# Kernel optimization log

Measured on AMD Instinct MI355X. Metric: run time of the kernel, lower is better.

## Reference

```python
import jax, jax.numpy as jnp
import numpy as np

NB, NG = 100000, 20000   # bus / gen node counts
D, H = 64, 64            # input feat dim, hidden dim
EL, EX = 1000000, 200000 # line edges, gen<->bus edges
OUT = 16


def setup_inputs() -> dict:
    key = jax.random.key(0)
    ks = jax.random.split(key, 28)

    def nrm(k, shp, scale):
        return jax.random.normal(k, shp, jnp.float32) * scale

    w = 0.05  # small weight scale to keep activations tame over stacked layers
    inp = {
        "x_bus": nrm(ks[0], (NB, D), 1.0),
        "x_gen": nrm(ks[1], (NG, D), 1.0),
        "line_src": jax.random.randint(ks[2], (EL,), 0, NB, jnp.int32),
        "line_dst": jax.random.randint(ks[3], (EL,), 0, NB, jnp.int32),
        "g2b_src": jax.random.randint(ks[4], (EX,), 0, NG, jnp.int32),
        "g2b_dst": jax.random.randint(ks[5], (EX,), 0, NB, jnp.int32),
        "b2g_src": jax.random.randint(ks[6], (EX,), 0, NB, jnp.int32),
        "b2g_dst": jax.random.randint(ks[7], (EX,), 0, NG, jnp.int32),
    }
    i = 8
    for l in range(2):
        din = D if l == 0 else H
        for name in ["W_self_bus", "W_self_gen", "W_line", "W_g2b", "W_b2g"]:
            inp[f"{name}_{l}"] = nrm(ks[i], (din, H), w); i += 1
        inp[f"b_self_bus_{l}"] = jnp.zeros((H,), jnp.float32)
        inp[f"b_self_gen_{l}"] = jnp.zeros((H,), jnp.float32)
    inp["W_h"] = nrm(ks[i], (2 * H, H), w); i += 1
    inp["b_h"] = jnp.zeros((H,), jnp.float32)
    inp["W_o"] = nrm(ks[i], (H, OUT), w); i += 1
    inp["b_o"] = jnp.zeros((OUT,), jnp.float32)
    return inp


def _mean_aggr(msg_src, src, dst, n_dst):
    # transform-at-source already applied; gather then mean-scatter to dst nodes
    m = msg_src[src]  # [E, H]
    s = jax.ops.segment_sum(m, dst, num_segments=n_dst)
    c = jax.ops.segment_sum(jnp.ones(dst.shape, m.dtype), dst, num_segments=n_dst)
    return s / jnp.maximum(c, 1.0)[:, None]


def reference(x_bus, x_gen, line_src, line_dst, g2b_src, g2b_dst, b2g_src, b2g_dst,
              W_self_bus_0, W_self_gen_0, W_line_0, W_g2b_0, W_b2g_0,
              b_self_bus_0, b_self_gen_0,
              W_self_bus_1, W_self_gen_1, W_line_1, W_g2b_1, W_b2g_1,
              b_self_bus_1, b_self_gen_1,
              W_h, b_h, W_o, b_o):
    layers = [
        (W_self_bus_0, b_self_bus_0, W_self_gen_0, b_self_gen_0, W_line_0, W_g2b_0, W_b2g_0),
        (W_self_bus_1, b_self_bus_1, W_self_gen_1, b_self_gen_1, W_line_1, W_g2b_1, W_b2g_1),
    ]
    hb, hg = x_bus, x_gen
    nb, ng = hb.shape[0], hg.shape[0]
    for (Wsb, bsb, Wsg, bsg, Wl, Wg2b, Wb2g) in layers:
        m_line = _mean_aggr(hb @ Wl, line_src, line_dst, nb)   # bus -> bus
        m_g2b = _mean_aggr(hg @ Wg2b, g2b_src, g2b_dst, nb)    # gen -> bus
        m_b2g = _mean_aggr(hb @ Wb2g, b2g_src, b2g_dst, ng)    # bus -> gen
        new_hb = jax.nn.relu(hb @ Wsb + bsb + m_line + m_g2b)
        new_hg = jax.nn.relu(hg @ Wsg + bsg + m_b2g)
        hb, hg = new_hb, new_hg
    # sum-pool each node type, concat, 2-layer MLP head
    g = jnp.concatenate([jnp.sum(hb, axis=0), jnp.sum(hg, axis=0)], axis=-1)
    return jax.nn.relu(g @ W_h + b_h) @ W_o + b_o
```

## Files before the change

kernel.cpp:

```cpp
#include <hip/hip_runtime.h>

#define NB 100000
#define NG 20000
#define EL 1000000
#define EX 200000
#define NSEG (2 * NB + NG)
#define NE (EL + 2 * EX)
#define WROW 72
#define WMAT (64 * WROW)
#define AST 200
#define FPB 128
#define PSEG (NSEG / 8)
#define CAPL 40
#define CAPG 16
#define CAPB 40

typedef __attribute__((ext_vector_type(8))) short bf16x8;
typedef __attribute__((ext_vector_type(4))) float f32x4;

static __device__ __forceinline__ int uni(int x) { return __builtin_amdgcn_readfirstlane(x); }

static __device__ __forceinline__ unsigned short f2bf(float x) {
    unsigned u = __float_as_uint(x);
    u += 0x7FFF + ((u >> 16) & 1);
    return (unsigned short)(u >> 16);
}
static __device__ __forceinline__ float bf2f(unsigned short s) {
    return __uint_as_float(((unsigned)s) << 16);
}

__global__ void cvt_kernel(const float* __restrict__ src, unsigned short* __restrict__ dst, int n) {
    int i = (blockIdx.x * blockDim.x + threadIdx.x) * 4;
    if (i < n) {
        float4 f = *(const float4*)(src + i);
        ushort4 u = { f2bf(f.x), f2bf(f.y), f2bf(f.z), f2bf(f.w) };
        *(ushort4*)(dst + i) = u;
    }
}

__global__ __launch_bounds__(256) void fill_bucket_kernel(
    const int* __restrict__ ls, const int* __restrict__ ld,
    const int* __restrict__ gs, const int* __restrict__ gd,
    const int* __restrict__ bs, const int* __restrict__ bd,
    int* __restrict__ cnt, int* __restrict__ bktL,
    int* __restrict__ bktG, int* __restrict__ bktB)
{
    const int p = blockIdx.x & 7;
    const int q = blockIdx.x >> 3;
    const int lo = p * PSEG;
    const int hi = lo + PSEG;
    for (int i = q * 256 + threadIdx.x; i < NE; i += FPB * 256) {
        int src, seg, cap;
        int* dst;
        if (i < EL) {
            src = ls[i]; int d = ld[i];
            seg = d; dst = bktL + (size_t)d * CAPL; cap = CAPL;
        } else if (i < EL + EX) {
            src = gs[i - EL]; int d = gd[i - EL];
            seg = NB + d; dst = bktG + (size_t)d * CAPG; cap = CAPG;
        } else {
            src = bs[i - EL - EX]; int d = bd[i - EL - EX];
            seg = 2 * NB + d; dst = bktB + (size_t)d * CAPB; cap = CAPB;
        }
        if (seg >= lo && seg < hi) {
            int pos = atomicAdd(&cnt[seg], 1);
            if (pos < cap) dst[pos] = src;
        }
    }
}

struct WPrep { const float* src[10]; unsigned short* dst[10]; };
__global__ __launch_bounds__(256) void wprep_kernel(WPrep p) {
    const float* __restrict__ s = p.src[blockIdx.x];
    unsigned short* __restrict__ d = p.dst[blockIdx.x];
    for (int idx = threadIdx.x; idx < 4096; idx += 256) {
        int k = idx >> 6, nn = idx & 63;
        d[nn * WROW + k] = f2bf(s[idx]);
    }
}

static __device__ __forceinline__ float seg_mean_bkt(const unsigned short* __restrict__ h,
                                                     const int* __restrict__ bkt,
                                                     int cnt, int cap, int lane) {
    float s = 0.f;
    const int n = min(cnt, cap);
    int e = 0;
    for (; e + 8 <= n; e += 8) {
        int i0 = bkt[e],     i1 = bkt[e + 1], i2 = bkt[e + 2], i3 = bkt[e + 3];
        int i4 = bkt[e + 4], i5 = bkt[e + 5], i6 = bkt[e + 6], i7 = bkt[e + 7];
        float v0 = bf2f(h[(size_t)i0 * 64 + lane]), v1 = bf2f(h[(size_t)i1 * 64 + lane]);
        float v2 = bf2f(h[(size_t)i2 * 64 + lane]), v3 = bf2f(h[(size_t)i3 * 64 + lane]);
        float v4 = bf2f(h[(size_t)i4 * 64 + lane]), v5 = bf2f(h[(size_t)i5 * 64 + lane]);
        float v6 = bf2f(h[(size_t)i6 * 64 + lane]), v7 = bf2f(h[(size_t)i7 * 64 + lane]);
        s += ((v0 + v1) + (v2 + v3)) + ((v4 + v5) + (v6 + v7));
    }
    for (; e + 2 <= n; e += 2) {
        int i0 = bkt[e], i1 = bkt[e + 1];
        s += bf2f(h[(size_t)i0 * 64 + lane]) + bf2f(h[(size_t)i1 * 64 + lane]);
    }
    if (e < n) s += bf2f(h[(size_t)bkt[e] * 64 + lane]);
    return s / fmaxf((float)cnt, 1.f);
}

__global__ __launch_bounds__(256) void combine_fused_kernel(
    const unsigned short* __restrict__ hb, const unsigned short* __restrict__ hg,
    const int* __restrict__ cnt,
    const int* __restrict__ bktL, const int* __restrict__ bktG, const int* __restrict__ bktB,
    const unsigned short* __restrict__ WtB, const unsigned short* __restrict__ WtG,
    const float* __restrict__ biasB, const float* __restrict__ biasG,
    unsigned short* __restrict__ outB, unsigned short* __restrict__ outG,
    float* __restrict__ pool, int gbBus)
{
    __shared__ __attribute__((aligned(16))) unsigned short Atile[32 * AST];
    __shared__ float pred[64];
    const int t = threadIdx.x;
    const bool isBus = blockIdx.x < gbBus;
    const int bb = isBus ? blockIdx.x : blockIdx.x - gbBus;
    const int base = bb * 32;
    const int n = isBus ? NB : NG;
    const int nmat = isBus ? 3 : 2;
    const unsigned short* __restrict__ h = isBus ? hb : hg;
    const unsigned short* __restrict__ Wt = isBus ? WtB : WtG;
    const float* __restrict__ bias = isBus ? biasB : biasG;

    if (pool != nullptr && t < 64) pred[t] = 0.f;

#pragma unroll
    for (int i = 0; i < 2; ++i) {
        int flat = i * 1024 + t * 4;
        int r = flat >> 6, c = flat & 63;
        bool ok = (base + r) < n;
        ushort4 z = {0, 0, 0, 0};
        size_t g = (size_t)(base + r) * 64 + c;
        *(ushort4*)&Atile[r * AST + c] = ok ? *(const ushort4*)(h + g) : z;
    }

    const int lane = t & 63;
    const int w = t >> 6;
    for (int r8 = 0; r8 < 8; ++r8) {
        const int r = w * 8 + r8;
        const int row = uni(base + r);
        float vA = 0.f, vB = 0.f;
        if (row < n) {
            if (isBus) {
                int cA = uni(cnt[row]);
                vA = seg_mean_bkt(hb, bktL + (size_t)row * CAPL, cA, CAPL, lane);
                int cB = uni(cnt[NB + row]);
                vB = seg_mean_bkt(hg, bktG + (size_t)row * CAPG, cB, CAPG, lane);
            } else {
                int cA = uni(cnt[2 * NB + row]);
                vA = seg_mean_bkt(hb, bktB + (size_t)row * CAPB, cA, CAPB, lane);
            }
        }
        Atile[r * AST + 64 + lane] = f2bf(vA);
        if (isBus) Atile[r * AST + 128 + lane] = f2bf(vB);
    }
    __syncthreads();

    const int rg = w & 1;
    const int cp = w >> 1;
    const int l15 = lane & 15;
    const int q = lane >> 4;
    f32x4 acc[2];
    acc[0] = (f32x4){0.f, 0.f, 0.f, 0.f};
    acc[1] = (f32x4){0.f, 0.f, 0.f, 0.f};

    const int ksteps = nmat * 2;
    for (int ks = 0; ks < ksteps; ++ks) {
        bf16x8 av = *(const bf16x8*)&Atile[(rg * 16 + l15) * AST + ks * 32 + q * 8];
#pragma unroll
        for (int cc = 0; cc < 2; ++cc) {
            int c = cp * 2 + cc;
            bf16x8 bv = *(const bf16x8*)&Wt[(ks >> 1) * WMAT + (c * 16 + l15) * WROW + (ks & 1) * 32 + q * 8];
            acc[cc] = __builtin_amdgcn_mfma_f32_16x16x32_bf16(av, bv, acc[cc], 0, 0, 0);
        }
    }

    if (pool == nullptr) {
        unsigned short* __restrict__ out = isBus ? outB : outG;
#pragma unroll
        for (int cc = 0; cc < 2; ++cc) {
            const int col = (cp * 2 + cc) * 16 + l15;
            const float bv = bias[col];
#pragma unroll
            for (int reg = 0; reg < 4; ++reg) {
                int row = base + rg * 16 + q * 4 + reg;
                if (row < n) out[(size_t)row * 64 + col] = f2bf(fmaxf(acc[cc][reg] + bv, 0.f));
            }
        }
    } else {
        float* __restrict__ pdst = isBus ? pool : pool + 64;
#pragma unroll
        for (int cc = 0; cc < 2; ++cc) {
            const int col = (cp * 2 + cc) * 16 + l15;
            const float bv = bias[col];
            float s = 0.f;
#pragma unroll
            for (int reg = 0; reg < 4; ++reg) {
                int row = base + rg * 16 + q * 4 + reg;
                if (row < n) s += fmaxf(acc[cc][reg] + bv, 0.f);
            }
            atomicAdd(&pred[col], s);
        }
        __syncthreads();
        if (t < 64) atomicAdd(&pdst[t], pred[t]);
    }
}

__global__ void head_kernel(const float* __restrict__ pool,
                            const float* __restrict__ Wh, const float* __restrict__ bh,
                            const float* __restrict__ Wo, const float* __restrict__ bo,
                            float* __restrict__ out)
{
    __shared__ float g[128];
    __shared__ float hid[64];
    int t = threadIdx.x;
    g[t] = pool[t];
    __syncthreads();
    if (t < 64) {
        float a = bh[t];
        for (int i = 0; i < 128; ++i) a += g[i] * Wh[i * 64 + t];
        hid[t] = fmaxf(a, 0.f);
    }
    __syncthreads();
    if (t < 16) {
        float a = bo[t];
        for (int j = 0; j < 64; ++j) a += hid[j] * Wo[j * 16 + t];
        out[t] = a;
    }
}

extern "C" void kernel_launch(void* const* d_in, const int* in_sizes, int n_in,
                              void* d_out, int out_size, void* d_ws, size_t ws_size,
                              hipStream_t stream)
{
    const float* x_bus   = (const float*)d_in[0];
    const float* x_gen   = (const float*)d_in[1];
    const int* line_src  = (const int*)d_in[2];
    const int* line_dst  = (const int*)d_in[3];
    const int* g2b_src   = (const int*)d_in[4];
    const int* g2b_dst   = (const int*)d_in[5];
    const int* b2g_src   = (const int*)d_in[6];
    const int* b2g_dst   = (const int*)d_in[7];
    const float* Wsb[2]  = {(const float*)d_in[8],  (const float*)d_in[15]};
    const float* Wsg[2]  = {(const float*)d_in[9],  (const float*)d_in[16]};
    const float* Wl[2]   = {(const float*)d_in[10], (const float*)d_in[17]};
    const float* Wg2b[2] = {(const float*)d_in[11], (const float*)d_in[18]};
    const float* Wb2g[2] = {(const float*)d_in[12], (const float*)d_in[19]};
    const float* bsb[2]  = {(const float*)d_in[13], (const float*)d_in[20]};
    const float* bsg[2]  = {(const float*)d_in[14], (const float*)d_in[21]};
    const float* Wh = (const float*)d_in[22];
    const float* bh = (const float*)d_in[23];
    const float* Wo = (const float*)d_in[24];
    const float* bo = (const float*)d_in[25];
    (void)in_sizes; (void)n_in; (void)out_size; (void)ws_size;

    char* wsB = (char*)d_ws;
    size_t o = 0;
    auto alloc_f = [&](size_t nelem) { o = (o + 15) & ~(size_t)15; float* p = (float*)(wsB + o); o += nelem * sizeof(float); return p; };
    auto alloc_i = [&](size_t nelem) { o = (o + 15) & ~(size_t)15; int* p = (int*)(wsB + o); o += nelem * sizeof(int); return p; };
    auto alloc_u = [&](size_t nelem) { o = (o + 15) & ~(size_t)15; unsigned short* p = (unsigned short*)(wsB + o); o += nelem * sizeof(unsigned short); return p; };

    unsigned short* xb16  = alloc_u((size_t)NB * 64);
    unsigned short* xg16  = alloc_u((size_t)NG * 64);
    unsigned short* H1b   = alloc_u((size_t)NB * 64);
    unsigned short* H1g   = alloc_u((size_t)NG * 64);
    int*   bktL = alloc_i((size_t)NB * CAPL);
    int*   bktG = alloc_i((size_t)NB * CAPG);
    int*   bktB = alloc_i((size_t)NG * CAPB);
    int*   cnt  = alloc_i(NSEG);
    float* pool = alloc_f(128);
    unsigned short* WtBus[2] = { alloc_u(3 * WMAT), alloc_u(3 * WMAT) };
    unsigned short* WtGen[2] = { alloc_u(2 * WMAT), alloc_u(2 * WMAT) };

    WPrep wp;
    for (int l = 0; l < 2; ++l) {
        wp.src[l * 5 + 0] = Wsb[l];  wp.dst[l * 5 + 0] = WtBus[l] + 0 * WMAT;
        wp.src[l * 5 + 1] = Wl[l];   wp.dst[l * 5 + 1] = WtBus[l] + 1 * WMAT;
        wp.src[l * 5 + 2] = Wg2b[l]; wp.dst[l * 5 + 2] = WtBus[l] + 2 * WMAT;
        wp.src[l * 5 + 3] = Wsg[l];  wp.dst[l * 5 + 3] = WtGen[l] + 0 * WMAT;
        wp.src[l * 5 + 4] = Wb2g[l]; wp.dst[l * 5 + 4] = WtGen[l] + 1 * WMAT;
    }
    wprep_kernel<<<10, 256, 0, stream>>>(wp);
    cvt_kernel<<<(NB * 64 / 4 + 255) / 256, 256, 0, stream>>>(x_bus, xb16, NB * 64);
    cvt_kernel<<<(NG * 64 / 4 + 255) / 256, 256, 0, stream>>>(x_gen, xg16, NG * 64);

    hipMemsetAsync(cnt, 0, NSEG * sizeof(int), stream);
    hipMemsetAsync(pool, 0, 128 * sizeof(float), stream);
    fill_bucket_kernel<<<8 * FPB, 256, 0, stream>>>(line_src, line_dst, g2b_src, g2b_dst,
                                                    b2g_src, b2g_dst, cnt, bktL, bktG, bktB);

    const int gbBus = NB / 32;
    const int gbGen = NG / 32;

    combine_fused_kernel<<<gbBus + gbGen, 256, 0, stream>>>(
        xb16, xg16, cnt, bktL, bktG, bktB, WtBus[0], WtGen[0], bsb[0], bsg[0],
        H1b, H1g, nullptr, gbBus);

    combine_fused_kernel<<<gbBus + gbGen, 256, 0, stream>>>(
        H1b, H1g, cnt, bktL, bktG, bktB, WtBus[1], WtGen[1], bsb[1], bsg[1],
        nullptr, nullptr, pool, gbBus);

    head_kernel<<<1, 128, 0, stream>>>(pool, Wh, bh, Wo, bo, (float*)d_out);
}
```

Measured before the change: 348.0 us.

## Gather neighbor features in fp8 and read fp32 self features directly

Neighbor-aggregation gathers now read a software fp8 (e4m3-like) copy of node features instead of bf16, halving the random-gather bytes. Layer 0 loads self features straight from fp32 and converts them in-kernel, so the bf16 conversion pass is no longer needed, and layer 1 writes both bf16 and fp8 outputs. Row bounds checks are dropped because node counts divide evenly by 32. The cost is lower precision in the aggregated messages, extra decode ALU work, and an extra fp8 write per layer.

After: 356.3 us. 2.4% more time.

```diff
diff --git a/kernel.cpp b/kernel.cpp
--- a/kernel.cpp
+++ b/kernel.cpp
@@ -25,16 +25,30 @@
     u += 0x7FFF + ((u >> 16) & 1);
     return (unsigned short)(u >> 16);
 }
-static __device__ __forceinline__ float bf2f(unsigned short s) {
-    return __uint_as_float(((unsigned)s) << 16);
-}
-
-__global__ void cvt_kernel(const float* __restrict__ src, unsigned short* __restrict__ dst, int n) {
+
+static __device__ __forceinline__ unsigned char ftofp8(float x) {
+    unsigned u = __float_as_uint(x);
+    unsigned sg = (u >> 24) & 0x80u;
+    unsigned mag = u & 0x7fffffffu;
+    mag += 0x7FFFFu + ((mag >> 20) & 1u);
+    int e = (int)(mag >> 23) - 120;
+    if (e <= 0) return (unsigned char)sg;
+    if (e > 15) return (unsigned char)(sg | 0x7E);
+    return (unsigned char)(sg | ((unsigned)e << 3) | ((mag >> 20) & 7u));
+}
+static __device__ __forceinline__ float fp8d(unsigned v) {
+    unsigned em = v & 0x7fu;
+    unsigned sg = (v & 0x80u) << 24;
+    float f = __uint_as_float(sg | ((em << 20) + 0x3C000000u));
+    return em < 8u ? __uint_as_float(sg) : f;
+}
+
+__global__ void cvt8_kernel(const float* __restrict__ src, unsigned char* __restrict__ dst, int n) {
     int i = (blockIdx.x * blockDim.x + threadIdx.x) * 4;
     if (i < n) {
         float4 f = *(const float4*)(src + i);
-        ushort4 u = { f2bf(f.x), f2bf(f.y), f2bf(f.z), f2bf(f.w) };
-        *(ushort4*)(dst + i) = u;
+        uchar4 u = { ftofp8(f.x), ftofp8(f.y), ftofp8(f.z), ftofp8(f.w) };
+        *(uchar4*)(dst + i) = u;
     }
 }
 
@@ -79,36 +93,40 @@
     }
 }
 
-static __device__ __forceinline__ float seg_mean_bkt(const unsigned short* __restrict__ h,
+static __device__ __forceinline__ float seg_mean_fp8(const unsigned char* __restrict__ h8,
                                                      const int* __restrict__ bkt,
-                                                     int cnt, int cap, int lane) {
+                                                     int c, int cap, int lane) {
     float s = 0.f;
-    const int n = min(cnt, cap);
+    const int n = min(c, cap);
     int e = 0;
     for (; e + 8 <= n; e += 8) {
         int i0 = bkt[e],     i1 = bkt[e + 1], i2 = bkt[e + 2], i3 = bkt[e + 3];
         int i4 = bkt[e + 4], i5 = bkt[e + 5], i6 = bkt[e + 6], i7 = bkt[e + 7];
-        float v0 = bf2f(h[(size_t)i0 * 64 + lane]), v1 = bf2f(h[(size_t)i1 * 64 + lane]);
-        float v2 = bf2f(h[(size_t)i2 * 64 + lane]), v3 = bf2f(h[(size_t)i3 * 64 + lane]);
-        float v4 = bf2f(h[(size_t)i4 * 64 + lane]), v5 = bf2f(h[(size_t)i5 * 64 + lane]);
-        float v6 = bf2f(h[(size_t)i6 * 64 + lane]), v7 = bf2f(h[(size_t)i7 * 64 + lane]);
-        s += ((v0 + v1) + (v2 + v3)) + ((v4 + v5) + (v6 + v7));
+        unsigned b0 = h8[(size_t)i0 * 64 + lane], b1 = h8[(size_t)i1 * 64 + lane];
+        unsigned b2 = h8[(size_t)i2 * 64 + lane], b3 = h8[(size_t)i3 * 64 + lane];
+        unsigned b4 = h8[(size_t)i4 * 64 + lane], b5 = h8[(size_t)i5 * 64 + lane];
+        unsigned b6 = h8[(size_t)i6 * 64 + lane], b7 = h8[(size_t)i7 * 64 + lane];
+        s += ((fp8d(b0) + fp8d(b1)) + (fp8d(b2) + fp8d(b3)))
+           + ((fp8d(b4) + fp8d(b5)) + (fp8d(b6) + fp8d(b7)));
     }
     for (; e + 2 <= n; e += 2) {
         int i0 = bkt[e], i1 = bkt[e + 1];
-        s += bf2f(h[(size_t)i0 * 64 + lane]) + bf2f(h[(size_t)i1 * 64 + lane]);
-    }
-    if (e < n) s += bf2f(h[(size_t)bkt[e] * 64 + lane]);
-    return s / fmaxf((float)cnt, 1.f);
+        s += fp8d(h8[(size_t)i0 * 64 + lane]) + fp8d(h8[(size_t)i1 * 64 + lane]);
+    }
+    if (e < n) s += fp8d(h8[(size_t)bkt[e] * 64 + lane]);
+    return s / fmaxf((float)c, 1.f);
 }
 
 __global__ __launch_bounds__(256) void combine_fused_kernel(
-    const unsigned short* __restrict__ hb, const unsigned short* __restrict__ hg,
+    const float* __restrict__ sFb, const float* __restrict__ sFg,
+    const unsigned short* __restrict__ sBb, const unsigned short* __restrict__ sBg,
+    const unsigned char* __restrict__ h8b, const unsigned char* __restrict__ h8g,
     const int* __restrict__ cnt,
     const int* __restrict__ bktL, const int* __restrict__ bktG, const int* __restrict__ bktB,
     const unsigned short* __restrict__ WtB, const unsigned short* __restrict__ WtG,
     const float* __restrict__ biasB, const float* __restrict__ biasG,
     unsigned short* __restrict__ outB, unsigned short* __restrict__ outG,
+    unsigned char* __restrict__ out8B, unsigned char* __restrict__ out8G,
     float* __restrict__ pool, int gbBus)
 {
     __shared__ __attribute__((aligned(16))) unsigned short Atile[32 * AST];
@@ -117,22 +135,27 @@
     const bool isBus = blockIdx.x < gbBus;
     const int bb = isBus ? blockIdx.x : blockIdx.x - gbBus;
     const int base = bb * 32;
-    const int n = isBus ? NB : NG;
-    const int nmat = isBus ? 3 : 2;
-    const unsigned short* __restrict__ h = isBus ? hb : hg;
-    const unsigned short* __restrict__ Wt = isBus ? WtB : WtG;
-    const float* __restrict__ bias = isBus ? biasB : biasG;
 
     if (pool != nullptr && t < 64) pred[t] = 0.f;
 
-#pragma unroll
-    for (int i = 0; i < 2; ++i) {
-        int flat = i * 1024 + t * 4;
-        int r = flat >> 6, c = flat & 63;
-        bool ok = (base + r) < n;
-        ushort4 z = {0, 0, 0, 0};
-        size_t g = (size_t)(base + r) * 64 + c;
-        *(ushort4*)&Atile[r * AST + c] = ok ? *(const ushort4*)(h + g) : z;
+    if (sFb != nullptr) {
+        const float* __restrict__ sf = isBus ? sFb : sFg;
+#pragma unroll
+        for (int i = 0; i < 2; ++i) {
+            int flat = i * 1024 + t * 4;
+            int r = flat >> 6, c = flat & 63;
+            float4 f = *(const float4*)(sf + (size_t)(base + r) * 64 + c);
+            ushort4 u = { f2bf(f.x), f2bf(f.y), f2bf(f.z), f2bf(f.w) };
+            *(ushort4*)&Atile[r * AST + c] = u;
+        }
+    } else {
+        const unsigned short* __restrict__ sb = isBus ? sBb : sBg;
+#pragma unroll
+        for (int i = 0; i < 2; ++i) {
+            int flat = i * 1024 + t * 4;
+            int r = flat >> 6, c = flat & 63;
+            *(ushort4*)&Atile[r * AST + c] = *(const ushort4*)(sb + (size_t)(base + r) * 64 + c);
+        }
     }
 
     const int lane = t & 63;
@@ -140,23 +163,24 @@
     for (int r8 = 0; r8 < 8; ++r8) {
         const int r = w * 8 + r8;
         const int row = uni(base + r);
-        float vA = 0.f, vB = 0.f;
-        if (row < n) {
-            if (isBus) {
-                int cA = uni(cnt[row]);
-                vA = seg_mean_bkt(hb, bktL + (size_t)row * CAPL, cA, CAPL, lane);
-                int cB = uni(cnt[NB + row]);
-                vB = seg_mean_bkt(hg, bktG + (size_t)row * CAPG, cB, CAPG, lane);
-            } else {
-                int cA = uni(cnt[2 * NB + row]);
-                vA = seg_mean_bkt(hb, bktB + (size_t)row * CAPB, cA, CAPB, lane);
-            }
-        }
-        Atile[r * AST + 64 + lane] = f2bf(vA);
-        if (isBus) Atile[r * AST + 128 + lane] = f2bf(vB);
+        if (isBus) {
+            int cA = uni(cnt[row]);
+            float vA = seg_mean_fp8(h8b, bktL + (size_t)row * CAPL, cA, CAPL, lane);
+            Atile[r * AST + 64 + lane] = f2bf(vA);
+            int cB = uni(cnt[NB + row]);
+            float vB = seg_mean_fp8(h8g, bktG + (size_t)row * CAPG, cB, CAPG, lane);
+            Atile[r * AST + 128 + lane] = f2bf(vB);
+        } else {
+            int cA = uni(cnt[2 * NB + row]);
+            float vA = seg_mean_fp8(h8b, bktB + (size_t)row * CAPB, cA, CAPB, lane);
+            Atile[r * AST + 64 + lane] = f2bf(vA);
+        }
     }
     __syncthreads();
 
+    const int nmat = isBus ? 3 : 2;
+    const unsigned short* __restrict__ Wt = isBus ? WtB : WtG;
+    const float* __restrict__ bias = isBus ? biasB : biasG;
     const int rg = w & 1;
     const int cp = w >> 1;
     const int l15 = lane & 15;
@@ -178,6 +202,7 @@
 
     if (pool == nullptr) {
         unsigned short* __restrict__ out = isBus ? outB : outG;
+        unsigned char* __restrict__ o8 = isBus ? out8B : out8G;
 #pragma unroll
         for (int cc = 0; cc < 2; ++cc) {
             const int col = (cp * 2 + cc) * 16 + l15;
@@ -185,7 +210,9 @@
 #pragma unroll
             for (int reg = 0; reg < 4; ++reg) {
                 int row = base + rg * 16 + q * 4 + reg;
-                if (row < n) out[(size_t)row * 64 + col] = f2bf(fmaxf(acc[cc][reg] + bv, 0.f));
+                float val = fmaxf(acc[cc][reg] + bv, 0.f);
+                out[(size_t)row * 64 + col] = f2bf(val);
+                o8[(size_t)row * 64 + col] = ftofp8(val);
             }
         }
     } else {
@@ -197,8 +224,7 @@
             float s = 0.f;
 #pragma unroll
             for (int reg = 0; reg < 4; ++reg) {
-                int row = base + rg * 16 + q * 4 + reg;
-                if (row < n) s += fmaxf(acc[cc][reg] + bv, 0.f);
+                s += fmaxf(acc[cc][reg] + bv, 0.f);
             }
             atomicAdd(&pred[col], s);
         }
@@ -260,11 +286,14 @@
     auto alloc_f = [&](size_t nelem) { o = (o + 15) & ~(size_t)15; float* p = (float*)(wsB + o); o += nelem * sizeof(float); return p; };
     auto alloc_i = [&](size_t nelem) { o = (o + 15) & ~(size_t)15; int* p = (int*)(wsB + o); o += nelem * sizeof(int); return p; };
     auto alloc_u = [&](size_t nelem) { o = (o + 15) & ~(size_t)15; unsigned short* p = (unsigned short*)(wsB + o); o += nelem * sizeof(unsigned short); return p; };
-
-    unsigned short* xb16  = alloc_u((size_t)NB * 64);
-    unsigned short* xg16  = alloc_u((size_t)NG * 64);
-    unsigned short* H1b   = alloc_u((size_t)NB * 64);
-    unsigned short* H1g   = alloc_u((size_t)NG * 64);
+    auto alloc_b = [&](size_t nelem) { o = (o + 15) & ~(size_t)15; unsigned char* p = (unsigned char*)(wsB + o); o += nelem; return p; };
+
+    unsigned short* H1b  = alloc_u((size_t)NB * 64);
+    unsigned short* H1g  = alloc_u((size_t)NG * 64);
+    unsigned char* xb8   = alloc_b((size_t)NB * 64);
+    unsigned char* xg8   = alloc_b((size_t)NG * 64);
+    unsigned char* H1b8  = alloc_b((size_t)NB * 64);
+    unsigned char* H1g8  = alloc_b((size_t)NG * 64);
     int*   bktL = alloc_i((size_t)NB * CAPL);
     int*   bktG = alloc_i((size_t)NB * CAPG);
     int*   bktB = alloc_i((size_t)NG * CAPB);
@@ -282,8 +311,8 @@
         wp.src[l * 5 + 4] = Wb2g[l]; wp.dst[l * 5 + 4] = WtGen[l] + 1 * WMAT;
     }
     wprep_kernel<<<10, 256, 0, stream>>>(wp);
-    cvt_kernel<<<(NB * 64 / 4 + 255) / 256, 256, 0, stream>>>(x_bus, xb16, NB * 64);
-    cvt_kernel<<<(NG * 64 / 4 + 255) / 256, 256, 0, stream>>>(x_gen, xg16, NG * 64);
+    cvt8_kernel<<<(NB * 64 / 4 + 255) / 256, 256, 0, stream>>>(x_bus, xb8, NB * 64);
+    cvt8_kernel<<<(NG * 64 / 4 + 255) / 256, 256, 0, stream>>>(x_gen, xg8, NG * 64);
 
     hipMemsetAsync(cnt, 0, NSEG * sizeof(int), stream);
     hipMemsetAsync(pool, 0, 128 * sizeof(float), stream);
@@ -294,12 +323,14 @@
     const int gbGen = NG / 32;
 
     combine_fused_kernel<<<gbBus + gbGen, 256, 0, stream>>>(
-        xb16, xg16, cnt, bktL, bktG, bktB, WtBus[0], WtGen[0], bsb[0], bsg[0],
-        H1b, H1g, nullptr, gbBus);
+        x_bus, x_gen, nullptr, nullptr, xb8, xg8,
+        cnt, bktL, bktG, bktB, WtBus[0], WtGen[0], bsb[0], bsg[0],
+        H1b, H1g, H1b8, H1g8, nullptr, gbBus);
 
     combine_fused_kernel<<<gbBus + gbGen, 256, 0, stream>>>(
-        H1b, H1g, cnt, bktL, bktG, bktB, WtBus[1], WtGen[1], bsb[1], bsg[1],
-        nullptr, nullptr, pool, gbBus);
+        nullptr, nullptr, H1b, H1g, H1b8, H1g8,
+        cnt, bktL, bktG, bktB, WtBus[1], WtGen[1], bsb[1], bsg[1],
+        nullptr, nullptr, nullptr, nullptr, pool, gbBus);
 
     head_kernel<<<1, 128, 0, stream>>>(pool, Wh, bh, Wo, bo, (float*)d_out);
 }
```
